# Optimization experiments

Measured on AMD Instinct MI355X. Metric: run time of the kernel, lower is better.

## Reference

```python
import jax, jax.numpy as jnp
import numpy as np

N_NODES = 100000
N_EDGES = 1600000
F = 64          # node_features (in == out for EvolveGCNO)
HID = 64        # hidden_size


def setup_inputs() -> dict:
    key = jax.random.key(0)
    ks = jax.random.split(key, 12)
    s = 1.0 / np.sqrt(F)
    inp = {
        "x": jax.random.normal(ks[0], (N_NODES, F), dtype=jnp.float32),
        "edge_index": jax.random.randint(ks[1], (2, N_EDGES), 0, N_NODES, dtype=jnp.int64),
        "edge_weight": jax.random.uniform(ks[2], (N_EDGES,), dtype=jnp.float32),
        # evolving GCN weight (initial_weight of EvolveGCNO)
        "W0": jax.random.uniform(ks[3], (F, F), jnp.float32, -s, s),
        # GRU (input_size=F, hidden_size=F): gates ordered r, z, n
        "gru_Wi": jax.random.uniform(ks[4], (3 * F, F), jnp.float32, -s, s),
        "gru_Wh": jax.random.uniform(ks[5], (3 * F, F), jnp.float32, -s, s),
        "gru_bi": jax.random.uniform(ks[6], (3 * F,), jnp.float32, -s, s),
        "gru_bh": jax.random.uniform(ks[7], (3 * F,), jnp.float32, -s, s),
        # projection F -> HID and head HID -> 1
        "proj_W": jax.random.uniform(ks[8], (HID, F), jnp.float32, -s, s),
        "proj_b": jax.random.uniform(ks[9], (HID,), jnp.float32, -s, s),
        "lin_W": jax.random.uniform(ks[10], (1, HID), jnp.float32, -1.0 / np.sqrt(HID), 1.0 / np.sqrt(HID)),
        "lin_b": jax.random.uniform(ks[11], (1,), jnp.float32, -1.0 / np.sqrt(HID), 1.0 / np.sqrt(HID)),
    }
    return inp


def reference(x, edge_index, edge_weight, W0, gru_Wi, gru_Wh, gru_bi, gru_bh,
              proj_W, proj_b, lin_W, lin_b):
    N = x.shape[0]
    # --- EvolveGCNO weight evolution: one GRU step, rows of W0 are both input and hidden ---
    gi = W0 @ gru_Wi.T + gru_bi  # [F, 3F]
    gh = W0 @ gru_Wh.T + gru_bh  # [F, 3F]
    i_r, i_z, i_n = jnp.split(gi, 3, axis=1)
    h_r, h_z, h_n = jnp.split(gh, 3, axis=1)
    r = jax.nn.sigmoid(i_r + h_r)
    z = jax.nn.sigmoid(i_z + h_z)
    n = jnp.tanh(i_n + r * h_n)
    W = (1.0 - z) * n + z * W0  # evolved GCN weight [F, F]

    # --- GCNConv with fixed evolved W: X' = D^-1/2 (A + I) D^-1/2 (X W) ---
    xw = x @ W  # [N, F]
    src, dst = edge_index[0], edge_index[1]
    loop = jnp.arange(N)
    src2 = jnp.concatenate([src, loop])
    dst2 = jnp.concatenate([dst, loop])
    w2 = jnp.concatenate([edge_weight, jnp.ones((N,), xw.dtype)])  # self-loop weight 1
    deg = jax.ops.segment_sum(w2, dst2, num_segments=N)
    dinv = jnp.where(deg > 0, jax.lax.rsqrt(deg), 0.0)
    norm = dinv[src2] * w2 * dinv[dst2]  # [E + N]
    h = jax.ops.segment_sum(xw[src2] * norm[:, None], dst2, num_segments=N)  # [N, F]

    # --- MLP head (dropout is identity in eval) ---
    h = jax.nn.relu(h @ proj_W.T + proj_b)
    return h @ lin_W.T + lin_b  # [N, 1]
```

## Files before the change

kernel.cpp:

```cpp
#include <hip/hip_runtime.h>
#include <stdint.h>

#define FDIM 64
#define BINSH 6
#define NBINS 1563
#define BCAP 1536
#define OVCAP 8192
#define PSTAGE 8192
#define PBLK 196
#define LSTRIDE 72

__device__ __forceinline__ float bf2f(unsigned int u) {
    union { float f; uint32_t i; } v; v.i = (u & 0xFFFFu) << 16; return v.f;
}
__device__ __forceinline__ unsigned short f2bf(float f) {
    union { float f; uint32_t i; } v; v.f = f;
    uint32_t u = v.i;
    u += 0x7FFFu + ((u >> 16) & 1u);
    return (unsigned short)(u >> 16);
}

__global__ __launch_bounds__(256) void k_sentinel(float* out, int N, float val) {
    int n = blockIdx.x * 256 + threadIdx.x;
    if (n < N) out[n] = (n == 0) ? val : 0.f;
}

__global__ __launch_bounds__(1024) void k_prep(
    const int* __restrict__ src, const int* __restrict__ dst,
    const float* __restrict__ ew, int* __restrict__ gcnt,
    int2* __restrict__ part, int* __restrict__ ovf_cnt,
    int* __restrict__ ovs, int* __restrict__ ovd, float* __restrict__ ovw, int E,
    const float* __restrict__ W0, const float* __restrict__ Wi,
    const float* __restrict__ Wh, const float* __restrict__ bi,
    const float* __restrict__ bh, const float* __restrict__ projW,
    float* __restrict__ M) {
    __shared__ int2 sorted_[PSTAGE];
    __shared__ int  gposa[PSTAGE];
    __shared__ int  hist[NBINS];
    __shared__ int  lbase[NBINS];
    __shared__ int  lcur[NBINS];
    __shared__ int  gboff[NBINS];
    __shared__ int  wsum[16];
    int t = threadIdx.x;
    if (blockIdx.x < PBLK) {
        for (int b = t; b < NBINS; b += 1024) hist[b] = 0;
        __syncthreads();
        int e0 = blockIdx.x * PSTAGE;
        int cnt = E - e0; if (cnt > PSTAGE) cnt = PSTAGE;
        int   d_r[8], s_r[8];
        float w_r[8];
#pragma unroll
        for (int k = 0; k < 8; k++) {
            int i = t + (k << 10);
            if (i < cnt) {
                int e = e0 + i;
                d_r[k] = dst[e]; s_r[k] = src[e]; w_r[k] = ew[e];
            }
        }
#pragma unroll
        for (int k = 0; k < 8; k++) {
            int i = t + (k << 10);
            if (i < cnt) atomicAdd(&hist[d_r[k] >> BINSH], 1);
        }
        __syncthreads();
        for (int b = t; b < NBINS; b += 1024) {
            int h = hist[b];
            gboff[b] = h ? atomicAdd(&gcnt[b], h) : 0;
        }
        int b0i = 2 * t, b1i = 2 * t + 1;
        int h0 = (b0i < NBINS) ? hist[b0i] : 0;
        int h1 = (b1i < NBINS) ? hist[b1i] : 0;
        int c2 = h0 + h1;
        int lane = t & 63, wid = t >> 6;
        int v = c2;
#pragma unroll
        for (int d = 1; d < 64; d <<= 1) {
            int o = __shfl_up(v, d);
            if (lane >= d) v += o;
        }
        if (lane == 63) wsum[wid] = v;
        __syncthreads();
        if (t < 16) {
            int w = wsum[t];
#pragma unroll
            for (int d = 1; d < 16; d <<= 1) {
                int o = __shfl_up(w, d);
                if (t >= d) w += o;
            }
            wsum[t] = w;
        }
        __syncthreads();
        int base = (wid > 0) ? wsum[wid - 1] : 0;
        int excl = base + v - c2;
        if (b0i < NBINS) { lbase[b0i] = excl;      lcur[b0i] = excl; }
        if (b1i < NBINS) { lbase[b1i] = excl + h0; lcur[b1i] = excl + h0; }
        __syncthreads();
#pragma unroll
        for (int k = 0; k < 8; k++) {
            int i = t + (k << 10);
            if (i < cnt) {
                int d = d_r[k];
                int b = d >> BINSH;
                int p = atomicAdd(&lcur[b], 1);
                sorted_[p] = make_int2(s_r[k] | ((d & 63) << 20), __float_as_int(w_r[k]));
                int off = gboff[b] + (p - lbase[b]);
                if (off < BCAP) {
                    gposa[p] = b * BCAP + off;
                } else {
                    gposa[p] = -1;
                    int op = atomicAdd(ovf_cnt, 1);
                    if (op < OVCAP) { ovs[op] = s_r[k]; ovd[op] = d; ovw[op] = w_r[k]; }
                }
            }
        }
        __syncthreads();
        for (int j = t; j < cnt; j += 1024) {
            int g = gposa[j];
            if (g >= 0) part[g] = sorted_[j];
        }
    } else {
        int i = blockIdx.x - PBLK;
        float* w0s  = (float*)sorted_;
        float* wrow = w0s + 64;
        if (t < 64) w0s[t] = W0[i * 64 + t];
        __syncthreads();
        if (t < 64) {
            int j = t;
            float a0 = 0.f, a1 = 0.f, a2 = 0.f, b0 = 0.f, b1 = 0.f, b2 = 0.f;
#pragma unroll 8
            for (int k = 0; k < 64; k++) {
                float w0k = w0s[k];
                a0 += w0k * Wi[(j)       * 64 + k];
                a1 += w0k * Wi[(64 + j)  * 64 + k];
                a2 += w0k * Wi[(128 + j) * 64 + k];
                b0 += w0k * Wh[(j)       * 64 + k];
                b1 += w0k * Wh[(64 + j)  * 64 + k];
                b2 += w0k * Wh[(128 + j) * 64 + k];
            }
            float ir = a0 + bi[j],        hr = b0 + bh[j];
            float iz = a1 + bi[64 + j],   hz = b1 + bh[64 + j];
            float in_ = a2 + bi[128 + j], hn = b2 + bh[128 + j];
            float r = 1.f / (1.f + expf(-(ir + hr)));
            float z = 1.f / (1.f + expf(-(iz + hz)));
            float n = tanhf(in_ + r * hn);
            wrow[j] = (1.f - z) * n + z * w0s[j];
        }
        __syncthreads();
        if (t < 64) {
            float s = 0.f;
#pragma unroll 8
            for (int q = 0; q < 64; q++) s += wrow[q] * projW[t * 64 + q];
            M[i * 64 + t] = s;
        }
    }
}

__global__ __launch_bounds__(256) void k_xmdeg(
    const float* __restrict__ x, const float* __restrict__ M,
    unsigned short* __restrict__ xm, int N,
    const int* __restrict__ gcnt, const int2* __restrict__ part,
    const int* __restrict__ ovf_cnt, const int* __restrict__ ovd,
    const float* __restrict__ ovw, float* __restrict__ dinv,
    int* __restrict__ loffg) {
    __shared__ char sm[34816];
    int t = threadIdx.x;
    if (blockIdx.x < NBINS) {
        float* xs = (float*)sm;
        float* ms = xs + 64 * 68;
        int nb = blockIdx.x * 64;
#pragma unroll
        for (int i = 0; i < 4; i++) {
            int lin = i * 1024 + t * 4;
            int row = lin >> 6, col = lin & 63;
            int node = nb + row;
            float4 v = make_float4(0.f, 0.f, 0.f, 0.f);
            if (node < N) v = *(const float4*)(x + (size_t)node * 64 + col);
            *(float4*)&xs[row * 68 + col] = v;
            *(float4*)&ms[row * 68 + col] = *(const float4*)(M + lin);
        }
        __syncthreads();
        int tj = t & 15, tn = t >> 4;
        float acc[4][4] = {};
        for (int k = 0; k < 64; k += 4) {
            float4 xv[4], mv[4];
#pragma unroll
            for (int nn = 0; nn < 4; nn++) xv[nn] = *(const float4*)&xs[(tn * 4 + nn) * 68 + k];
#pragma unroll
            for (int kk = 0; kk < 4; kk++) mv[kk] = *(const float4*)&ms[(k + kk) * 68 + tj * 4];
#pragma unroll
            for (int nn = 0; nn < 4; nn++) {
                const float* xp = (const float*)&xv[nn];
#pragma unroll
                for (int kk = 0; kk < 4; kk++) {
                    float xk = xp[kk];
                    const float* mp = (const float*)&mv[kk];
                    acc[nn][0] += xk * mp[0];
                    acc[nn][1] += xk * mp[1];
                    acc[nn][2] += xk * mp[2];
                    acc[nn][3] += xk * mp[3];
                }
            }
        }
#pragma unroll
        for (int nn = 0; nn < 4; nn++) {
            int node = nb + tn * 4 + nn;
            if (node < N) {
                ushort4 o;
                o.x = f2bf(acc[nn][0]); o.y = f2bf(acc[nn][1]);
                o.z = f2bf(acc[nn][2]); o.w = f2bf(acc[nn][3]);
                *(ushort4*)&xm[(size_t)node * 64 + tj * 4] = o;
            }
        }
    } else {
        int b = blockIdx.x - NBINS;
        float* dl   = (float*)sm;
        int*   cntl = (int*)(dl + 64);
        int*   lofl = cntl + 64;
        if (t < 64) { dl[t] = 1.0f; cntl[t] = 0; }
        __syncthreads();
        int c = gcnt[b]; if (c > BCAP) c = BCAP;
        const int2* pe = part + (size_t)b * BCAP;
        for (int i = t; i < c; i += 256) {
            int2 e = pe[i];
            int nl = (e.x >> 20) & 63;
            atomicAdd(&dl[nl], __int_as_float(e.y));
            atomicAdd(&cntl[nl], 1);
        }
        int m = *ovf_cnt; if (m > OVCAP) m = OVCAP;
        for (int i = t; i < m; i += 256) {
            int d = ovd[i];
            if ((d >> BINSH) == b) atomicAdd(&dl[d & 63], ovw[i]);
        }
        __syncthreads();
        if (t == 0) {
            int o = 0;
#pragma unroll 16
            for (int k = 0; k < 64; k++) { lofl[k] = o; o += cntl[k]; }
            lofl[64] = o;
        }
        __syncthreads();
        if (t < 64) {
            int n = b * 64 + t;
            if (n < N) dinv[n] = rsqrtf(dl[t]);
        }
        if (t < 65) loffg[b * LSTRIDE + t] = lofl[t];
    }
}

__global__ __launch_bounds__(512) void k_gf(
    const unsigned short* __restrict__ xm, const float* __restrict__ dinv,
    const int* __restrict__ gcnt, const int2* __restrict__ part,
    const int* __restrict__ loffg,
    const float* __restrict__ projB, const float* __restrict__ linW,
    const float* __restrict__ linB, const int* __restrict__ ovf_cnt,
    const int* __restrict__ ovs, const int* __restrict__ ovd,
    const float* __restrict__ ovw, float* __restrict__ out, int N) {
    __shared__ int  loff[65];
    __shared__ int  lcur[64];
    __shared__ int2 ledge[BCAP];
    __shared__ float pbs[64], lws[64];
    int t = threadIdx.x, b = blockIdx.x;
    if (t < 65) loff[t] = loffg[b * LSTRIDE + t];
    if (t < 64) { pbs[t] = projB[t]; lws[t] = linW[t]; }
    __syncthreads();
    if (t < 64) lcur[t] = loff[t];
    __syncthreads();
    int c = gcnt[b]; if (c > BCAP) c = BCAP;
    const int2* pe = part + (size_t)b * BCAP;
    for (int i = t; i < c; i += 512) {
        int2 e = pe[i];
        int s = e.x & 0xFFFFF;
        float nw = dinv[s] * __int_as_float(e.y);
        int p = atomicAdd(&lcur[(e.x >> 20) & 63], 1);
        ledge[p] = make_int2(e.x, __float_as_int(nw));
    }
    __syncthreads();
    int m = *ovf_cnt; if (m > OVCAP) m = OVCAP;
    float lb = linB[0];
    int wv = t >> 6, lane = t & 63, eg = lane >> 4, fq = lane & 15, f = fq * 4;
    for (int nl = wv; nl < 64; nl += 8) {
        int n = b * 64 + nl;
        if (n >= N) continue;
        float dn = dinv[n];
        int beg = loff[nl], end = loff[nl + 1];
        float a0 = 0.f, a1 = 0.f, a2 = 0.f, a3 = 0.f;
        float b0 = 0.f, b1 = 0.f, b2 = 0.f, b3 = 0.f;
        float c0 = 0.f, c1 = 0.f, c2 = 0.f, c3 = 0.f;
        float d0 = 0.f, d1 = 0.f, d2 = 0.f, d3 = 0.f;
        int i = beg + eg;
        for (; i + 12 < end; i += 16) {
            int2 e0 = ledge[i];
            int2 e1 = ledge[i + 4];
            int2 e2 = ledge[i + 8];
            int2 e3 = ledge[i + 12];
            uint2 u0 = *(const uint2*)&xm[(size_t)(e0.x & 0xFFFFF) * 64 + f];
            uint2 u1 = *(const uint2*)&xm[(size_t)(e1.x & 0xFFFFF) * 64 + f];
            uint2 u2 = *(const uint2*)&xm[(size_t)(e2.x & 0xFFFFF) * 64 + f];
            uint2 u3 = *(const uint2*)&xm[(size_t)(e3.x & 0xFFFFF) * 64 + f];
            float w0 = __int_as_float(e0.y);
            float w1 = __int_as_float(e1.y);
            float w2 = __int_as_float(e2.y);
            float w3 = __int_as_float(e3.y);
            a0 += w0 * bf2f(u0.x); a1 += w0 * bf2f(u0.x >> 16);
            a2 += w0 * bf2f(u0.y); a3 += w0 * bf2f(u0.y >> 16);
            b0 += w1 * bf2f(u1.x); b1 += w1 * bf2f(u1.x >> 16);
            b2 += w1 * bf2f(u1.y); b3 += w1 * bf2f(u1.y >> 16);
            c0 += w2 * bf2f(u2.x); c1 += w2 * bf2f(u2.x >> 16);
            c2 += w2 * bf2f(u2.y); c3 += w2 * bf2f(u2.y >> 16);
            d0 += w3 * bf2f(u3.x); d1 += w3 * bf2f(u3.x >> 16);
            d2 += w3 * bf2f(u3.y); d3 += w3 * bf2f(u3.y >> 16);
        }
        for (; i + 4 < end; i += 8) {
            int2 e0 = ledge[i];
            int2 e1 = ledge[i + 4];
            uint2 u0 = *(const uint2*)&xm[(size_t)(e0.x & 0xFFFFF) * 64 + f];
            uint2 u1 = *(const uint2*)&xm[(size_t)(e1.x & 0xFFFFF) * 64 + f];
            float w0 = __int_as_float(e0.y);
            float w1 = __int_as_float(e1.y);
            a0 += w0 * bf2f(u0.x); a1 += w0 * bf2f(u0.x >> 16);
            a2 += w0 * bf2f(u0.y); a3 += w0 * bf2f(u0.y >> 16);
            b0 += w1 * bf2f(u1.x); b1 += w1 * bf2f(u1.x >> 16);
            b2 += w1 * bf2f(u1.y); b3 += w1 * bf2f(u1.y >> 16);
        }
        for (; i < end; i += 4) {
            int2 e0 = ledge[i];
            uint2 u0 = *(const uint2*)&xm[(size_t)(e0.x & 0xFFFFF) * 64 + f];
            float w0 = __int_as_float(e0.y);
            a0 += w0 * bf2f(u0.x); a1 += w0 * bf2f(u0.x >> 16);
            a2 += w0 * bf2f(u0.y); a3 += w0 * bf2f(u0.y >> 16);
        }
        a0 += b0 + c0 + d0; a1 += b1 + c1 + d1;
        a2 += b2 + c2 + d2; a3 += b3 + c3 + d3;
        a0 *= dn; a1 *= dn; a2 *= dn; a3 *= dn;
        a0 += __shfl_xor(a0, 16); a1 += __shfl_xor(a1, 16);
        a2 += __shfl_xor(a2, 16); a3 += __shfl_xor(a3, 16);
        a0 += __shfl_xor(a0, 32); a1 += __shfl_xor(a1, 32);
        a2 += __shfl_xor(a2, 32); a3 += __shfl_xor(a3, 32);
        if (eg == 0) {
            {
                uint2 u = *(const uint2*)&xm[(size_t)n * 64 + f];
                float sl = dn * dn;
                a0 += sl * bf2f(u.x); a1 += sl * bf2f(u.x >> 16);
                a2 += sl * bf2f(u.y); a3 += sl * bf2f(u.y >> 16);
            }
            for (int q = 0; q < m; q++) {
                if (ovd[q] == n) {
                    int s = ovs[q];
                    float nm = dinv[s] * ovw[q] * dn;
                    uint2 u = *(const uint2*)&xm[(size_t)s * 64 + f];
                    a0 += nm * bf2f(u.x); a1 += nm * bf2f(u.x >> 16);
                    a2 += nm * bf2f(u.y); a3 += nm * bf2f(u.y >> 16);
                }
            }
            float v0 = a0 + pbs[f],     v1 = a1 + pbs[f + 1];
            float v2 = a2 + pbs[f + 2], v3 = a3 + pbs[f + 3];
            float s = (v0 > 0.f ? v0 : 0.f) * lws[f]
                    + (v1 > 0.f ? v1 : 0.f) * lws[f + 1]
                    + (v2 > 0.f ? v2 : 0.f) * lws[f + 2]
                    + (v3 > 0.f ? v3 : 0.f) * lws[f + 3];
            s += __shfl_xor(s, 1); s += __shfl_xor(s, 2);
            s += __shfl_xor(s, 4); s += __shfl_xor(s, 8);
            if (fq == 0) out[n] = s + lb;
        }
    }
}

extern "C" void kernel_launch(void* const* d_in, const int* in_sizes, int n_in,
                              void* d_out, int out_size, void* d_ws, size_t ws_size,
                              hipStream_t stream) {
    const float* x   = (const float*)d_in[0];
    const int*   ei  = (const int*)d_in[1];
    const float* ew  = (const float*)d_in[2];
    const float* W0  = (const float*)d_in[3];
    const float* gWi = (const float*)d_in[4];
    const float* gWh = (const float*)d_in[5];
    const float* gbi = (const float*)d_in[6];
    const float* gbh = (const float*)d_in[7];
    const float* pW  = (const float*)d_in[8];
    const float* pb  = (const float*)d_in[9];
    const float* lW  = (const float*)d_in[10];
    const float* lb  = (const float*)d_in[11];
    float* out = (float*)d_out;

    static const int EXPSZ[12] = {6400000, 3200000, 1600000, 4096, 12288, 12288,
                                  192, 192, 4096, 64, 64, 1};
    int mism = -1;
    for (int i = 0; i < 12 && i < n_in; i++)
        if (in_sizes[i] != EXPSZ[i]) { mism = i; break; }
    if (mism >= 0) {
        k_sentinel<<<(out_size + 255) / 256, 256, 0, stream>>>(out, out_size,
                                                               ldexpf(1.f, 30 + 3 * mism));
        return;
    }

    int N = in_sizes[0] / FDIM;
    int E = in_sizes[1] / 2;
    const int* src = ei;
    const int* dst = ei + E;

    char* wsb = (char*)d_ws;
    float* M       = (float*)(wsb);
    int*   gcnt    = (int*)  (wsb + (32u << 10));
    int*   ovf_cnt = (int*)  (wsb + (39u << 10));
    int*   ovs     = (int*)  (wsb + (44u << 10));
    int*   ovd     = (int*)  (wsb + (76u << 10));
    float* ovw     = (float*)(wsb + (108u << 10));
    float* dinv    = (float*)(wsb + (1u << 20));
    int*   loffg   = (int*)  (wsb + 1572864u);
    int2*  part    = (int2*) (wsb + (2u << 20));
    unsigned short* xm = (unsigned short*)(wsb + (22u << 20));

    hipMemsetAsync(gcnt, 0, (8u << 10), stream);

    k_prep<<<PBLK + 64, 1024, 0, stream>>>(src, dst, ew, gcnt, part,
                                           ovf_cnt, ovs, ovd, ovw, E,
                                           W0, gWi, gWh, gbi, gbh, pW, M);
    k_xmdeg<<<NBINS * 2, 256, 0, stream>>>(x, M, xm, N, gcnt, part,
                                           ovf_cnt, ovd, ovw, dinv, loffg);
    k_gf<<<NBINS, 512, 0, stream>>>(xm, dinv, gcnt, part, loffg, pb, lW, lb,
                                    ovf_cnt, ovs, ovd, ovw, out, N);
}
```

Measured before the change: 188.0 us.

## Replace per-node edge sort with shared-memory atomic feature accumulation in gather

The gather kernel no longer sorts each bin's edges into per-node segments using offsets computed in the degree kernel. Instead each 16-thread group processes one edge and atomically adds its weighted bf16 feature row into a padded shared-memory accumulator per local node. The degree pass drops its count and prefix-scan work, and the final head reads the accumulator directly. This trades the register-unrolled segmented reduction for many shared-memory float atomics, which may contend when several edges in a bin share a destination.

New measurement: 736.3 us. 292% more time.

```diff
diff --git a/kernel.cpp b/kernel.cpp
--- a/kernel.cpp
+++ b/kernel.cpp
@@ -8,7 +8,7 @@
 #define OVCAP 8192
 #define PSTAGE 8192
 #define PBLK 196
-#define LSTRIDE 72
+#define ASTR 65
 
 __device__ __forceinline__ float bf2f(unsigned int u) {
     union { float f; uint32_t i; } v; v.i = (u & 0xFFFFu) << 16; return v.f;
@@ -160,8 +160,7 @@
     unsigned short* __restrict__ xm, int N,
     const int* __restrict__ gcnt, const int2* __restrict__ part,
     const int* __restrict__ ovf_cnt, const int* __restrict__ ovd,
-    const float* __restrict__ ovw, float* __restrict__ dinv,
-    int* __restrict__ loffg) {
+    const float* __restrict__ ovw, float* __restrict__ dinv) {
     __shared__ char sm[34816];
     int t = threadIdx.x;
     if (blockIdx.x < NBINS) {
@@ -213,18 +212,14 @@
         }
     } else {
         int b = blockIdx.x - NBINS;
-        float* dl   = (float*)sm;
-        int*   cntl = (int*)(dl + 64);
-        int*   lofl = cntl + 64;
-        if (t < 64) { dl[t] = 1.0f; cntl[t] = 0; }
+        float* dl = (float*)sm;
+        if (t < 64) dl[t] = 1.0f;
         __syncthreads();
         int c = gcnt[b]; if (c > BCAP) c = BCAP;
         const int2* pe = part + (size_t)b * BCAP;
         for (int i = t; i < c; i += 256) {
             int2 e = pe[i];
-            int nl = (e.x >> 20) & 63;
-            atomicAdd(&dl[nl], __int_as_float(e.y));
-            atomicAdd(&cntl[nl], 1);
+            atomicAdd(&dl[(e.x >> 20) & 63], __int_as_float(e.y));
         }
         int m = *ovf_cnt; if (m > OVCAP) m = OVCAP;
         for (int i = t; i < m; i += 256) {
@@ -232,136 +227,63 @@
             if ((d >> BINSH) == b) atomicAdd(&dl[d & 63], ovw[i]);
         }
         __syncthreads();
-        if (t == 0) {
-            int o = 0;
-#pragma unroll 16
-            for (int k = 0; k < 64; k++) { lofl[k] = o; o += cntl[k]; }
-            lofl[64] = o;
-        }
-        __syncthreads();
         if (t < 64) {
             int n = b * 64 + t;
             if (n < N) dinv[n] = rsqrtf(dl[t]);
         }
-        if (t < 65) loffg[b * LSTRIDE + t] = lofl[t];
     }
 }
 
 __global__ __launch_bounds__(512) void k_gf(
     const unsigned short* __restrict__ xm, const float* __restrict__ dinv,
     const int* __restrict__ gcnt, const int2* __restrict__ part,
-    const int* __restrict__ loffg,
     const float* __restrict__ projB, const float* __restrict__ linW,
     const float* __restrict__ linB, const int* __restrict__ ovf_cnt,
     const int* __restrict__ ovs, const int* __restrict__ ovd,
     const float* __restrict__ ovw, float* __restrict__ out, int N) {
-    __shared__ int  loff[65];
-    __shared__ int  lcur[64];
-    __shared__ int2 ledge[BCAP];
+    __shared__ float accs[64 * ASTR];
     __shared__ float pbs[64], lws[64];
     int t = threadIdx.x, b = blockIdx.x;
-    if (t < 65) loff[t] = loffg[b * LSTRIDE + t];
     if (t < 64) { pbs[t] = projB[t]; lws[t] = linW[t]; }
-    __syncthreads();
-    if (t < 64) lcur[t] = loff[t];
+    for (int i = t; i < 64 * ASTR; i += 512) accs[i] = 0.f;
     __syncthreads();
     int c = gcnt[b]; if (c > BCAP) c = BCAP;
     const int2* pe = part + (size_t)b * BCAP;
-    for (int i = t; i < c; i += 512) {
+    int fq = t & 15, f = fq * 4, gid = t >> 4;
+    for (int i = gid; i < c; i += 32) {
         int2 e = pe[i];
         int s = e.x & 0xFFFFF;
+        int nl = (e.x >> 20) & 63;
         float nw = dinv[s] * __int_as_float(e.y);
-        int p = atomicAdd(&lcur[(e.x >> 20) & 63], 1);
-        ledge[p] = make_int2(e.x, __float_as_int(nw));
+        uint2 u = *(const uint2*)&xm[(size_t)s * 64 + f];
+        float* ap = &accs[nl * ASTR + f];
+        atomicAdd(ap + 0, nw * bf2f(u.x));
+        atomicAdd(ap + 1, nw * bf2f(u.x >> 16));
+        atomicAdd(ap + 2, nw * bf2f(u.y));
+        atomicAdd(ap + 3, nw * bf2f(u.y >> 16));
     }
     __syncthreads();
     int m = *ovf_cnt; if (m > OVCAP) m = OVCAP;
     float lb = linB[0];
-    int wv = t >> 6, lane = t & 63, eg = lane >> 4, fq = lane & 15, f = fq * 4;
+    int wv = t >> 6, lane = t & 63;
     for (int nl = wv; nl < 64; nl += 8) {
         int n = b * 64 + nl;
         if (n >= N) continue;
         float dn = dinv[n];
-        int beg = loff[nl], end = loff[nl + 1];
-        float a0 = 0.f, a1 = 0.f, a2 = 0.f, a3 = 0.f;
-        float b0 = 0.f, b1 = 0.f, b2 = 0.f, b3 = 0.f;
-        float c0 = 0.f, c1 = 0.f, c2 = 0.f, c3 = 0.f;
-        float d0 = 0.f, d1 = 0.f, d2 = 0.f, d3 = 0.f;
-        int i = beg + eg;
-        for (; i + 12 < end; i += 16) {
-            int2 e0 = ledge[i];
-            int2 e1 = ledge[i + 4];
-            int2 e2 = ledge[i + 8];
-            int2 e3 = ledge[i + 12];
-            uint2 u0 = *(const uint2*)&xm[(size_t)(e0.x & 0xFFFFF) * 64 + f];
-            uint2 u1 = *(const uint2*)&xm[(size_t)(e1.x & 0xFFFFF) * 64 + f];
-            uint2 u2 = *(const uint2*)&xm[(size_t)(e2.x & 0xFFFFF) * 64 + f];
-            uint2 u3 = *(const uint2*)&xm[(size_t)(e3.x & 0xFFFFF) * 64 + f];
-            float w0 = __int_as_float(e0.y);
-            float w1 = __int_as_float(e1.y);
-            float w2 = __int_as_float(e2.y);
-            float w3 = __int_as_float(e3.y);
-            a0 += w0 * bf2f(u0.x); a1 += w0 * bf2f(u0.x >> 16);
-            a2 += w0 * bf2f(u0.y); a3 += w0 * bf2f(u0.y >> 16);
-            b0 += w1 * bf2f(u1.x); b1 += w1 * bf2f(u1.x >> 16);
-            b2 += w1 * bf2f(u1.y); b3 += w1 * bf2f(u1.y >> 16);
-            c0 += w2 * bf2f(u2.x); c1 += w2 * bf2f(u2.x >> 16);
-            c2 += w2 * bf2f(u2.y); c3 += w2 * bf2f(u2.y >> 16);
-            d0 += w3 * bf2f(u3.x); d1 += w3 * bf2f(u3.x >> 16);
-            d2 += w3 * bf2f(u3.y); d3 += w3 * bf2f(u3.y >> 16);
-        }
-        for (; i + 4 < end; i += 8) {
-            int2 e0 = ledge[i];
-            int2 e1 = ledge[i + 4];
-            uint2 u0 = *(const uint2*)&xm[(size_t)(e0.x & 0xFFFFF) * 64 + f];
-            uint2 u1 = *(const uint2*)&xm[(size_t)(e1.x & 0xFFFFF) * 64 + f];
-            float w0 = __int_as_float(e0.y);
-            float w1 = __int_as_float(e1.y);
-            a0 += w0 * bf2f(u0.x); a1 += w0 * bf2f(u0.x >> 16);
-            a2 += w0 * bf2f(u0.y); a3 += w0 * bf2f(u0.y >> 16);
-            b0 += w1 * bf2f(u1.x); b1 += w1 * bf2f(u1.x >> 16);
-            b2 += w1 * bf2f(u1.y); b3 += w1 * bf2f(u1.y >> 16);
-        }
-        for (; i < end; i += 4) {
-            int2 e0 = ledge[i];
-            uint2 u0 = *(const uint2*)&xm[(size_t)(e0.x & 0xFFFFF) * 64 + f];
-            float w0 = __int_as_float(e0.y);
-            a0 += w0 * bf2f(u0.x); a1 += w0 * bf2f(u0.x >> 16);
-            a2 += w0 * bf2f(u0.y); a3 += w0 * bf2f(u0.y >> 16);
-        }
-        a0 += b0 + c0 + d0; a1 += b1 + c1 + d1;
-        a2 += b2 + c2 + d2; a3 += b3 + c3 + d3;
-        a0 *= dn; a1 *= dn; a2 *= dn; a3 *= dn;
-        a0 += __shfl_xor(a0, 16); a1 += __shfl_xor(a1, 16);
-        a2 += __shfl_xor(a2, 16); a3 += __shfl_xor(a3, 16);
-        a0 += __shfl_xor(a0, 32); a1 += __shfl_xor(a1, 32);
-        a2 += __shfl_xor(a2, 32); a3 += __shfl_xor(a3, 32);
-        if (eg == 0) {
-            {
-                uint2 u = *(const uint2*)&xm[(size_t)n * 64 + f];
-                float sl = dn * dn;
-                a0 += sl * bf2f(u.x); a1 += sl * bf2f(u.x >> 16);
-                a2 += sl * bf2f(u.y); a3 += sl * bf2f(u.y >> 16);
-            }
-            for (int q = 0; q < m; q++) {
-                if (ovd[q] == n) {
-                    int s = ovs[q];
-                    float nm = dinv[s] * ovw[q] * dn;
-                    uint2 u = *(const uint2*)&xm[(size_t)s * 64 + f];
-                    a0 += nm * bf2f(u.x); a1 += nm * bf2f(u.x >> 16);
-                    a2 += nm * bf2f(u.y); a3 += nm * bf2f(u.y >> 16);
-                }
-            }
-            float v0 = a0 + pbs[f],     v1 = a1 + pbs[f + 1];
-            float v2 = a2 + pbs[f + 2], v3 = a3 + pbs[f + 3];
-            float s = (v0 > 0.f ? v0 : 0.f) * lws[f]
-                    + (v1 > 0.f ? v1 : 0.f) * lws[f + 1]
-                    + (v2 > 0.f ? v2 : 0.f) * lws[f + 2]
-                    + (v3 > 0.f ? v3 : 0.f) * lws[f + 3];
-            s += __shfl_xor(s, 1); s += __shfl_xor(s, 2);
-            s += __shfl_xor(s, 4); s += __shfl_xor(s, 8);
-            if (fq == 0) out[n] = s + lb;
-        }
+        float a = accs[nl * ASTR + lane] * dn;
+        a += dn * dn * bf2f((unsigned int)xm[(size_t)n * 64 + lane]);
+        for (int q = 0; q < m; q++) {
+            if (ovd[q] == n) {
+                int s = ovs[q];
+                a += dinv[s] * ovw[q] * dn * bf2f((unsigned int)xm[(size_t)s * 64 + lane]);
+            }
+        }
+        float v = a + pbs[lane];
+        float s = (v > 0.f ? v : 0.f) * lws[lane];
+        s += __shfl_xor(s, 1);  s += __shfl_xor(s, 2);
+        s += __shfl_xor(s, 4);  s += __shfl_xor(s, 8);
+        s += __shfl_xor(s, 16); s += __shfl_xor(s, 32);
+        if (lane == 0) out[n] = s + lb;
     }
 }
 
@@ -406,7 +328,6 @@
     int*   ovd     = (int*)  (wsb + (76u << 10));
     float* ovw     = (float*)(wsb + (108u << 10));
     float* dinv    = (float*)(wsb + (1u << 20));
-    int*   loffg   = (int*)  (wsb + 1572864u);
     int2*  part    = (int2*) (wsb + (2u << 20));
     unsigned short* xm = (unsigned short*)(wsb + (22u << 20));
 
@@ -416,7 +337,7 @@
                                            ovf_cnt, ovs, ovd, ovw, E,
                                            W0, gWi, gWh, gbi, gbh, pW, M);
     k_xmdeg<<<NBINS * 2, 256, 0, stream>>>(x, M, xm, N, gcnt, part,
-                                           ovf_cnt, ovd, ovw, dinv, loffg);
-    k_gf<<<NBINS, 512, 0, stream>>>(xm, dinv, gcnt, part, loffg, pb, lW, lb,
+                                           ovf_cnt, ovd, ovw, dinv);
+    k_gf<<<NBINS, 512, 0, stream>>>(xm, dinv, gcnt, part, pb, lW, lb,
                                     ovf_cnt, ovs, ovd, ovw, out, N);
 }
```
